# Performance work log

Measured on AMD Instinct MI355X. Metric: run time of the kernel, lower is better.

The kernel has to match this reference:

```python
import jax, jax.numpy as jnp
import numpy as np
import math

DIM = 1024
NUMHEADS = 16
HEAD_DIM = DIM // NUMHEADS
B, N = 4, 1024


def setup_inputs() -> dict:
    key = jax.random.key(0)
    ks = jax.random.split(key, 12)
    x = jax.random.normal(ks[0], (B, N, DIM), dtype=jnp.float32)
    decaymask = jax.random.uniform(ks[1], (NUMHEADS, N, N), dtype=jnp.float32)
    s = 1.0 / math.sqrt(DIM)
    wq = jax.random.normal(ks[2], (DIM, DIM), dtype=jnp.float32) * s
    bq = jnp.zeros((DIM,), dtype=jnp.float32)
    wk = jax.random.normal(ks[3], (DIM, DIM), dtype=jnp.float32) * s
    bk = jnp.zeros((DIM,), dtype=jnp.float32)
    wv = jax.random.normal(ks[4], (DIM, DIM), dtype=jnp.float32) * s
    bv = jnp.zeros((DIM,), dtype=jnp.float32)
    wo = jax.random.normal(ks[5], (DIM, DIM), dtype=jnp.float32) * s
    bo = jnp.zeros((DIM,), dtype=jnp.float32)
    return {"x": x, "decaymask": decaymask, "wq": wq, "bq": bq, "wk": wk,
            "bk": bk, "wv": wv, "bv": bv, "wo": wo, "bo": bo}


def reference(x, decaymask, wq, bq, wk, bk, wv, bv, wo, bo):
    Bx, Nx, D = x.shape
    # projections (torch Linear: x @ W^T + b)
    q = x @ wq.T + bq
    k = x @ wk.T + bk
    v = x @ wv.T + bv
    # [B, H, N, Hd]
    q = q.reshape(Bx, Nx, NUMHEADS, HEAD_DIM).transpose(0, 2, 1, 3)
    k = k.reshape(Bx, Nx, NUMHEADS, HEAD_DIM).transpose(0, 2, 1, 3)
    v = v.reshape(Bx, Nx, NUMHEADS, HEAD_DIM).transpose(0, 2, 1, 3)
    scores = jnp.einsum('bhqd,bhkd->bhqk', q, k) / math.sqrt(HEAD_DIM)
    scores = scores * decaymask[None]  # multiplicative decay mask before softmax
    attn = jax.nn.softmax(scores, axis=-1)
    out = jnp.einsum('bhqk,bhkd->bhqd', attn, v)
    out = out.transpose(0, 2, 1, 3).reshape(Bx, Nx, D)
    return out @ wo.T + bo
```

## Files before the change

### kernel.cpp

```cpp
#include <hip/hip_runtime.h>
#include <hip/hip_bf16.h>
#include <math.h>

typedef __bf16 bf16;
typedef __bf16 bf16x8 __attribute__((ext_vector_type(8)));
typedef __bf16 bf16x4 __attribute__((ext_vector_type(4)));
typedef float f32x4 __attribute__((ext_vector_type(4)));
typedef unsigned short u16;
typedef u16 u16x8 __attribute__((ext_vector_type(8)));

#define SEQ 1024
#define DIMSZ 1024
#define NHEADS 16
#define HEADDIM 64
#define BATCH 4

typedef __attribute__((address_space(1))) const unsigned char gas_u8;
typedef __attribute__((address_space(3))) unsigned char las_u8;
__device__ __forceinline__ void gload16(const void* g, void* l) {
    __builtin_amdgcn_global_load_lds((const gas_u8*)g, (las_u8*)l, 16, 0, 0);
}

__global__ void cvt_swz(const float4* __restrict__ src, bf16* __restrict__ dst,
                        int n4, float scale) {
    int i = blockIdx.x * blockDim.x + threadIdx.x;
    if (i >= n4) return;
    float4 v = src[i];
    int e0 = i << 2;
    int row = e0 >> 10, col = e0 & 1023;
    int col2 = (col & ~63) | (col & 7) | (((((col >> 3) & 7) ^ (row & 7))) << 3);
    bf16x4 o;
    o[0] = (bf16)(v.x * scale);
    o[1] = (bf16)(v.y * scale);
    o[2] = (bf16)(v.z * scale);
    o[3] = (bf16)(v.w * scale);
    *reinterpret_cast<bf16x4*>(&dst[(size_t)row * 1024 + col2]) = o;
}

__device__ __forceinline__ bf16x8 fragswz(const bf16* base, int row, int kb) {
    return *reinterpret_cast<const bf16x8*>(
        reinterpret_cast<const char*>(base) + row * 128 + (kb ^ ((row & 7) << 4)));
}

#define LDT 72
__device__ __forceinline__ bf16x8 ldsfrag72(const bf16* base, int row0, int k0, int lane) {
    return *reinterpret_cast<const bf16x8*>(base + (row0 + (lane & 15)) * LDT + k0 + ((lane >> 4) << 3));
}

template <int WN, int OUT_F32>
__global__ __launch_bounds__(256) void gemm_glds(
    const bf16* __restrict__ A, const bf16* __restrict__ Bm,
    const float* __restrict__ b0, const float* __restrict__ b1, const float* __restrict__ b2,
    float s0, void* __restrict__ Cv, int M, int N, int K)
{
    __shared__ __align__(16) bf16 As[128 * 64];
    __shared__ __align__(16) bf16 Bs[WN * 32 * 64];

    const int BN = WN * 32;
    const int nbn = N / BN;
    const int bm = blockIdx.x / nbn, bn = blockIdx.x % nbn;
    const int m0 = bm << 7, n0 = bn * BN;
    const int tid = threadIdx.x, lane = tid & 63, wid = tid >> 6;
    const int wr = wid >> 1, wc = wid & 1;
    const int lq = lane & 15, g = lane >> 4;

    f32x4 acc[4][WN];
    #pragma unroll
    for (int m = 0; m < 4; ++m)
        #pragma unroll
        for (int n = 0; n < WN; ++n)
            acc[m][n] = (f32x4){0.f, 0.f, 0.f, 0.f};

    for (int kt = 0; kt < K; kt += 64) {
        #pragma unroll
        for (int i = 0; i < 4; ++i) {
            int rb = wid * 32 + i * 8;
            gload16(&A[(size_t)(m0 + rb + (lane >> 3)) * K + kt + ((lane & 7) << 3)],
                    &As[rb * 64]);
        }
        #pragma unroll
        for (int i = 0; i < WN; ++i) {
            int rb = wid * (WN * 8) + i * 8;
            gload16(&Bm[(size_t)(n0 + rb + (lane >> 3)) * K + kt + ((lane & 7) << 3)],
                    &Bs[rb * 64]);
        }
        __syncthreads();

        bf16x8 af[4][2], bfr[WN][2];
        #pragma unroll
        for (int m = 0; m < 4; ++m)
            #pragma unroll
            for (int h2 = 0; h2 < 2; ++h2)
                af[m][h2] = fragswz(As, wr * 64 + m * 16 + lq, h2 * 64 + g * 16);
        #pragma unroll
        for (int n = 0; n < WN; ++n)
            #pragma unroll
            for (int h2 = 0; h2 < 2; ++h2)
                bfr[n][h2] = fragswz(Bs, wc * (WN * 16) + n * 16 + lq, h2 * 64 + g * 16);

        #pragma unroll
        for (int m = 0; m < 4; ++m)
            #pragma unroll
            for (int n = 0; n < WN; ++n)
                #pragma unroll
                for (int h2 = 0; h2 < 2; ++h2)
                    acc[m][n] = __builtin_amdgcn_mfma_f32_16x16x32_bf16(
                        af[m][h2], bfr[n][h2], acc[m][n], 0, 0, 0);
        __syncthreads();
    }

    const int seg = n0 >> 10;
    const float* bp = (seg == 0) ? b0 : ((seg == 1) ? b1 : b2);
    const float bsc = (seg == 0) ? s0 : 1.f;

    #pragma unroll
    for (int m = 0; m < 4; ++m) {
        #pragma unroll
        for (int n = 0; n < WN; ++n) {
            int rbase = m0 + wr * 64 + m * 16 + (g << 2);
            int col = n0 + wc * (WN * 16) + n * 16 + lq;
            float bv = bp[col - (seg << 10)] * bsc;
            #pragma unroll
            for (int r = 0; r < 4; ++r) {
                float v = acc[m][n][r] + bv;
                if (OUT_F32)
                    ((float*)Cv)[(size_t)(rbase + r) * N + col] = v;
                else
                    ((bf16*)Cv)[(size_t)(rbase + r) * N + col] = (bf16)v;
            }
        }
    }
}

struct KVRegs { bf16x8 k0, k1; u16x8 v0, v1; };

__device__ __forceinline__ void issue_loads(KVRegs& r, const bf16* qkv, int brow,
                                            int koff, int voff, int tid) {
    const int rK = tid >> 3, o8 = (tid & 7) << 3;
    r.k0 = *reinterpret_cast<const bf16x8*>(&qkv[(size_t)(brow + rK) * 3072 + koff + o8]);
    r.k1 = *reinterpret_cast<const bf16x8*>(&qkv[(size_t)(brow + rK + 32) * 3072 + koff + o8]);
    const int rV = rK << 1;
    r.v0 = *reinterpret_cast<const u16x8*>(&qkv[(size_t)(brow + rV) * 3072 + voff + o8]);
    r.v1 = *reinterpret_cast<const u16x8*>(&qkv[(size_t)(brow + rV + 1) * 3072 + voff + o8]);
}

__device__ __forceinline__ void write_stage(const KVRegs& r, bf16* Kb, bf16* Vb, int tid) {
    const int rK = tid >> 3, o = tid & 7, o8 = o << 3;
    *reinterpret_cast<bf16x8*>(&Kb[rK * LDT + o8]) = r.k0;
    *reinterpret_cast<bf16x8*>(&Kb[(rK + 32) * LDT + o8]) = r.k1;
    const int rV = rK << 1;
    #pragma unroll
    for (int j = 0; j < 8; ++j) {
        int d = o8 + j;
        int byteo = (d * 144 + rV * 2) ^ (o << 4);
        unsigned int w = (unsigned int)r.v0[j] | ((unsigned int)r.v1[j] << 16);
        *reinterpret_cast<unsigned int*>(reinterpret_cast<char*>(Vb) + byteo) = w;
    }
}

__device__ __forceinline__ void compute_stage(
    const bf16* Kb, const bf16* Vb, bf16* Psw,
    const float4 (&mreg)[4], const bf16x8 (&aqb)[2],
    float& m_run, float& l_run, f32x4 (&oacc)[4], int lane)
{
    const int lq = lane & 15, g = lane >> 4;
    f32x4 sacc[4];
    #pragma unroll
    for (int ct = 0; ct < 4; ++ct) sacc[ct] = (f32x4){0.f, 0.f, 0.f, 0.f};
    #pragma unroll
    for (int ct = 0; ct < 4; ++ct)
        #pragma unroll
        for (int h2 = 0; h2 < 2; ++h2)
            sacc[ct] = __builtin_amdgcn_mfma_f32_16x16x32_bf16(
                ldsfrag72(Kb, ct * 16, h2 * 32, lane), aqb[h2], sacc[ct], 0, 0, 0);

    float sv[4][4];
    float mx = -3.0e38f;
    #pragma unroll
    for (int ct = 0; ct < 4; ++ct) {
        sv[ct][0] = sacc[ct][0] * mreg[ct].x;
        sv[ct][1] = sacc[ct][1] * mreg[ct].y;
        sv[ct][2] = sacc[ct][2] * mreg[ct].z;
        sv[ct][3] = sacc[ct][3] * mreg[ct].w;
        mx = fmaxf(mx, fmaxf(fmaxf(sv[ct][0], sv[ct][1]), fmaxf(sv[ct][2], sv[ct][3])));
    }
    mx = fmaxf(mx, __shfl_xor(mx, 16, 64));
    mx = fmaxf(mx, __shfl_xor(mx, 32, 64));

    if (!__all(mx <= m_run + 8.f)) {
        float mnew = fmaxf(m_run, mx);
        float scl = __expf(m_run - mnew);
        l_run *= scl;
        #pragma unroll
        for (int ot = 0; ot < 4; ++ot) oacc[ot] *= scl;
        m_run = mnew;
    }

    float sum = 0.f;
    float pl[4][4];
    #pragma unroll
    for (int ct = 0; ct < 4; ++ct)
        #pragma unroll
        for (int r = 0; r < 4; ++r) {
            float p = __expf(sv[ct][r] - m_run);
            pl[ct][r] = p;
            sum += p;
        }
    sum += __shfl_xor(sum, 16, 64);
    sum += __shfl_xor(sum, 32, 64);
    l_run += sum;

    #pragma unroll
    for (int ct = 0; ct < 4; ++ct) {
        bf16x4 pb;
        pb[0] = (bf16)pl[ct][0]; pb[1] = (bf16)pl[ct][1];
        pb[2] = (bf16)pl[ct][2]; pb[3] = (bf16)pl[ct][3];
        *reinterpret_cast<bf16x4*>(&Psw[lq * LDT + ct * 16 + (g << 2)]) = pb;
    }

    #pragma unroll
    for (int ot = 0; ot < 4; ++ot) {
        #pragma unroll
        for (int h2 = 0; h2 < 2; ++h2) {
            int d = ot * 16 + lq;
            int byteo = (d * 144 + (h2 * 32 + g * 8) * 2) ^ (((d >> 3) & 7) << 4);
            bf16x8 vf = *reinterpret_cast<const bf16x8*>(
                reinterpret_cast<const char*>(Vb) + byteo);
            bf16x8 pf = *reinterpret_cast<const bf16x8*>(&Psw[lq * LDT + h2 * 32 + g * 8]);
            oacc[ot] = __builtin_amdgcn_mfma_f32_16x16x32_bf16(vf, pf, oacc[ot], 0, 0, 0);
        }
    }
}

__global__ __launch_bounds__(256) void attn_kernel(
    const bf16* __restrict__ qkv, const float* __restrict__ mask, bf16* __restrict__ Og)
{
    __shared__ __align__(16) bf16 Kbuf[2][64 * LDT];
    __shared__ __align__(16) bf16 Vbuf[2][64 * LDT];
    __shared__ __align__(16) bf16 Ps[4][16 * LDT];

    const int bid = blockIdx.x;
    const int xcd = bid & 7, slot = bid >> 3;
    const int pg = xcd * 32 + (slot >> 1);
    const int bp = slot & 1;
    const int h = pg >> 4, qblk = pg & 15;

    const int tid = threadIdx.x, lane = tid & 63, wid = tid >> 6;
    const int lq = lane & 15, g = lane >> 4;
    const int q = (qblk << 6) + wid * 16 + lq;
    const int koff = 1024 + h * HEADDIM, voff = 2048 + h * HEADDIM, qoff = h * HEADDIM;
    const float* mh = mask + (size_t)h * SEQ * SEQ + (size_t)q * SEQ;

    bf16x8 aq[2][2];
    #pragma unroll
    for (int bi = 0; bi < 2; ++bi)
        #pragma unroll
        for (int h2 = 0; h2 < 2; ++h2)
            aq[bi][h2] = *reinterpret_cast<const bf16x8*>(
                &qkv[(size_t)((bp * 2 + bi) * SEQ + q) * 3072 + qoff + h2 * 32 + g * 8]);

    float m_run[2] = {-3.0e38f, -3.0e38f};
    float l_run[2] = {0.f, 0.f};
    f32x4 oacc[2][4] = {};

    KVRegs s0, s1;
    issue_loads(s0, qkv, (bp * 2 + 0) * SEQ, koff, voff, tid);
    issue_loads(s1, qkv, (bp * 2 + 1) * SEQ, koff, voff, tid);
    float4 mregA[4], mregB[4];
    #pragma unroll
    for (int ct = 0; ct < 4; ++ct) {
        mregA[ct] = *reinterpret_cast<const float4*>(&mh[ct * 16 + (g << 2)]);
        mregB[ct] = *reinterpret_cast<const float4*>(&mh[64 + ct * 16 + (g << 2)]);
    }
    write_stage(s0, Kbuf[0], Vbuf[0], tid);
    __syncthreads();

    for (int t = 0; t < 16; ++t) {
        if (t < 15) issue_loads(s0, qkv, (bp * 2 + 0) * SEQ + (t + 1) * 64, koff, voff, tid);
        compute_stage(Kbuf[0], Vbuf[0], Ps[wid], mregA, aq[0],
                      m_run[0], l_run[0], oacc[0], lane);
        write_stage(s1, Kbuf[1], Vbuf[1], tid);
        __syncthreads();

        if (t < 15) issue_loads(s1, qkv, (bp * 2 + 1) * SEQ + (t + 1) * 64, koff, voff, tid);
        compute_stage(Kbuf[1], Vbuf[1], Ps[wid], mregA, aq[1],
                      m_run[1], l_run[1], oacc[1], lane);
        #pragma unroll
        for (int ct = 0; ct < 4; ++ct) mregA[ct] = mregB[ct];
        if (t < 14)
            #pragma unroll
            for (int ct = 0; ct < 4; ++ct)
                mregB[ct] = *reinterpret_cast<const float4*>(&mh[(t + 2) * 64 + ct * 16 + (g << 2)]);
        if (t < 15) write_stage(s0, Kbuf[0], Vbuf[0], tid);
        __syncthreads();
    }

    #pragma unroll
    for (int bi = 0; bi < 2; ++bi) {
        float inv = 1.f / l_run[bi];
        #pragma unroll
        for (int ot = 0; ot < 4; ++ot) {
            bf16x4 o;
            o[0] = (bf16)(oacc[bi][ot][0] * inv);
            o[1] = (bf16)(oacc[bi][ot][1] * inv);
            o[2] = (bf16)(oacc[bi][ot][2] * inv);
            o[3] = (bf16)(oacc[bi][ot][3] * inv);
            int lcol = ot * 16 + (g << 2);
            int chunk = (lcol >> 3) ^ (q & 7);
            int col = h * HEADDIM + (chunk << 3) + (lcol & 7);
            *reinterpret_cast<bf16x4*>(
                &Og[(size_t)((bp * 2 + bi) * SEQ + q) * DIMSZ + col]) = o;
        }
    }
}

extern "C" void kernel_launch(void* const* d_in, const int* in_sizes, int n_in,
                              void* d_out, int out_size, void* d_ws, size_t ws_size,
                              hipStream_t stream) {
    const float* x    = (const float*)d_in[0];
    const float* mask = (const float*)d_in[1];
    const float* wq   = (const float*)d_in[2];
    const float* bq   = (const float*)d_in[3];
    const float* wk   = (const float*)d_in[4];
    const float* bk   = (const float*)d_in[5];
    const float* wv   = (const float*)d_in[6];
    const float* bv   = (const float*)d_in[7];
    const float* wo   = (const float*)d_in[8];
    const float* bo   = (const float*)d_in[9];
    float* out = (float*)d_out;

    const size_t MTOK = (size_t)BATCH * SEQ;
    char* ws = (char*)d_ws;
    bf16* xb    = (bf16*)ws; ws += MTOK * DIMSZ * 2;
    bf16* wqkvb = (bf16*)ws; ws += (size_t)3 * DIMSZ * DIMSZ * 2;
    bf16* wob   = (bf16*)ws; ws += (size_t)DIMSZ * DIMSZ * 2;
    bf16* qkv   = (bf16*)ws; ws += MTOK * 3 * DIMSZ * 2;
    bf16* aob   = (bf16*)ws; ws += MTOK * DIMSZ * 2;

    int n4x = (int)(MTOK * DIMSZ / 4);
    cvt_swz<<<(n4x + 255) / 256, 256, 0, stream>>>((const float4*)x, xb, n4x, 1.f);
    int n4w = DIMSZ * DIMSZ / 4;
    int gw = (n4w + 255) / 256;
    cvt_swz<<<gw, 256, 0, stream>>>((const float4*)wq, wqkvb,                 n4w, 0.125f);
    cvt_swz<<<gw, 256, 0, stream>>>((const float4*)wk, wqkvb + 1024 * 1024,   n4w, 1.f);
    cvt_swz<<<gw, 256, 0, stream>>>((const float4*)wv, wqkvb + 2 * 1024 * 1024, n4w, 1.f);
    cvt_swz<<<gw, 256, 0, stream>>>((const float4*)wo, wob,                   n4w, 1.f);

    gemm_glds<4, 0><<<(MTOK / 128) * (3 * DIMSZ / 128), 256, 0, stream>>>(
        xb, wqkvb, bq, bk, bv, 0.125f, qkv, (int)MTOK, 3 * DIMSZ, DIMSZ);

    attn_kernel<<<512, 256, 0, stream>>>(qkv, mask, aob);

    gemm_glds<2, 1><<<(MTOK / 128) * (DIMSZ / 64), 256, 0, stream>>>(
        aob, wob, bo, bo, bo, 1.f, out, (int)MTOK, DIMSZ, DIMSZ);
}
```

Measured before the change: 120.1 us.

## Restructure attention to 32 queries per wave, merge weight conversions, remap GEMM blocks

New measurement: 130.4 us. 1.09x slower.

```diff
diff --git a/kernel.cpp b/kernel.cpp
--- a/kernel.cpp
+++ b/kernel.cpp
@@ -21,12 +21,7 @@
     __builtin_amdgcn_global_load_lds((const gas_u8*)g, (las_u8*)l, 16, 0, 0);
 }
 
-__global__ void cvt_swz(const float4* __restrict__ src, bf16* __restrict__ dst,
-                        int n4, float scale) {
-    int i = blockIdx.x * blockDim.x + threadIdx.x;
-    if (i >= n4) return;
-    float4 v = src[i];
-    int e0 = i << 2;
+__device__ __forceinline__ void cvt_store(const float4 v, bf16* dst, int e0, float scale) {
     int row = e0 >> 10, col = e0 & 1023;
     int col2 = (col & ~63) | (col & 7) | (((((col >> 3) & 7) ^ (row & 7))) << 3);
     bf16x4 o;
@@ -37,6 +32,23 @@
     *reinterpret_cast<bf16x4*>(&dst[(size_t)row * 1024 + col2]) = o;
 }
 
+__global__ void cvt_swz(const float4* __restrict__ src, bf16* __restrict__ dst,
+                        int n4, float scale) {
+    int i = blockIdx.x * blockDim.x + threadIdx.x;
+    if (i >= n4) return;
+    cvt_store(src[i], dst, i << 2, scale);
+}
+
+__global__ void cvt_weights(const float4* __restrict__ wq, const float4* __restrict__ wk,
+                            const float4* __restrict__ wv, const float4* __restrict__ wo,
+                            bf16* __restrict__ wqkvb, bf16* __restrict__ wob) {
+    int i = blockIdx.x * blockDim.x + threadIdx.x;
+    int mat = i >> 18, li = i & 262143;
+    const float4* s = (mat == 0) ? wq : (mat == 1) ? wk : (mat == 2) ? wv : wo;
+    bf16* d = (mat < 3) ? (wqkvb + (size_t)mat * 1024 * 1024) : wob;
+    cvt_store(s[li], d, li << 2, (mat == 0) ? 0.125f : 1.f);
+}
+
 __device__ __forceinline__ bf16x8 fragswz(const bf16* base, int row, int kb) {
     return *reinterpret_cast<const bf16x8*>(
         reinterpret_cast<const char*>(base) + row * 128 + (kb ^ ((row & 7) << 4)));
@@ -58,7 +70,8 @@
 
     const int BN = WN * 32;
     const int nbn = N / BN;
-    const int bm = blockIdx.x / nbn, bn = blockIdx.x % nbn;
+    const int wrk = (blockIdx.x & 7) * ((int)gridDim.x >> 3) + (blockIdx.x >> 3);
+    const int bm = wrk / nbn, bn = wrk % nbn;
     const int m0 = bm << 7, n0 = bn * BN;
     const int tid = threadIdx.x, lane = tid & 63, wid = tid >> 6;
     const int wr = wid >> 1, wc = wid & 1;
@@ -98,6 +111,7 @@
             for (int h2 = 0; h2 < 2; ++h2)
                 bfr[n][h2] = fragswz(Bs, wc * (WN * 16) + n * 16 + lq, h2 * 64 + g * 16);
 
+        __builtin_amdgcn_s_setprio(1);
         #pragma unroll
         for (int m = 0; m < 4; ++m)
             #pragma unroll
@@ -106,6 +120,7 @@
                 for (int h2 = 0; h2 < 2; ++h2)
                     acc[m][n] = __builtin_amdgcn_mfma_f32_16x16x32_bf16(
                         af[m][h2], bfr[n][h2], acc[m][n], 0, 0, 0);
+        __builtin_amdgcn_s_setprio(0);
         __syncthreads();
     }
 
@@ -160,64 +175,86 @@
 
 __device__ __forceinline__ void compute_stage(
     const bf16* Kb, const bf16* Vb, bf16* Psw,
-    const float4 (&mreg)[4], const bf16x8 (&aqb)[2],
-    float& m_run, float& l_run, f32x4 (&oacc)[4], int lane)
+    const float4 (&mreg)[2][4], const bf16x8 (&aq)[2][2],
+    float (&m_run)[2], float (&l_run)[2], f32x4 (&oacc)[2][4], int lane)
 {
     const int lq = lane & 15, g = lane >> 4;
-    f32x4 sacc[4];
-    #pragma unroll
-    for (int ct = 0; ct < 4; ++ct) sacc[ct] = (f32x4){0.f, 0.f, 0.f, 0.f};
+
+    bf16x8 kf[4][2];
     #pragma unroll
     for (int ct = 0; ct < 4; ++ct)
         #pragma unroll
         for (int h2 = 0; h2 < 2; ++h2)
-            sacc[ct] = __builtin_amdgcn_mfma_f32_16x16x32_bf16(
-                ldsfrag72(Kb, ct * 16, h2 * 32, lane), aqb[h2], sacc[ct], 0, 0, 0);
-
-    float sv[4][4];
-    float mx = -3.0e38f;
-    #pragma unroll
-    for (int ct = 0; ct < 4; ++ct) {
-        sv[ct][0] = sacc[ct][0] * mreg[ct].x;
-        sv[ct][1] = sacc[ct][1] * mreg[ct].y;
-        sv[ct][2] = sacc[ct][2] * mreg[ct].z;
-        sv[ct][3] = sacc[ct][3] * mreg[ct].w;
-        mx = fmaxf(mx, fmaxf(fmaxf(sv[ct][0], sv[ct][1]), fmaxf(sv[ct][2], sv[ct][3])));
-    }
-    mx = fmaxf(mx, __shfl_xor(mx, 16, 64));
-    mx = fmaxf(mx, __shfl_xor(mx, 32, 64));
-
-    if (!__all(mx <= m_run + 8.f)) {
-        float mnew = fmaxf(m_run, mx);
-        float scl = __expf(m_run - mnew);
-        l_run *= scl;
-        #pragma unroll
-        for (int ot = 0; ot < 4; ++ot) oacc[ot] *= scl;
-        m_run = mnew;
-    }
-
-    float sum = 0.f;
-    float pl[4][4];
-    #pragma unroll
-    for (int ct = 0; ct < 4; ++ct)
-        #pragma unroll
-        for (int r = 0; r < 4; ++r) {
-            float p = __expf(sv[ct][r] - m_run);
-            pl[ct][r] = p;
-            sum += p;
-        }
-    sum += __shfl_xor(sum, 16, 64);
-    sum += __shfl_xor(sum, 32, 64);
-    l_run += sum;
-
-    #pragma unroll
-    for (int ct = 0; ct < 4; ++ct) {
-        bf16x4 pb;
-        pb[0] = (bf16)pl[ct][0]; pb[1] = (bf16)pl[ct][1];
-        pb[2] = (bf16)pl[ct][2]; pb[3] = (bf16)pl[ct][3];
-        *reinterpret_cast<bf16x4*>(&Psw[lq * LDT + ct * 16 + (g << 2)]) = pb;
-    }
-
+            kf[ct][h2] = ldsfrag72(Kb, ct * 16, h2 * 32, lane);
+
+    #pragma unroll
+    for (int qs = 0; qs < 2; ++qs) {
+        f32x4 sacc[4];
+        #pragma unroll
+        for (int ct = 0; ct < 4; ++ct) sacc[ct] = (f32x4){0.f, 0.f, 0.f, 0.f};
+        __builtin_amdgcn_s_setprio(1);
+        #pragma unroll
+        for (int ct = 0; ct < 4; ++ct)
+            #pragma unroll
+            for (int h2 = 0; h2 < 2; ++h2)
+                sacc[ct] = __builtin_amdgcn_mfma_f32_16x16x32_bf16(
+                    kf[ct][h2], aq[qs][h2], sacc[ct], 0, 0, 0);
+        __builtin_amdgcn_s_setprio(0);
+
+        float sv[4][4];
+        float mx = -3.0e38f;
+        #pragma unroll
+        for (int ct = 0; ct < 4; ++ct) {
+            sv[ct][0] = sacc[ct][0] * mreg[qs][ct].x;
+            sv[ct][1] = sacc[ct][1] * mreg[qs][ct].y;
+            sv[ct][2] = sacc[ct][2] * mreg[qs][ct].z;
+            sv[ct][3] = sacc[ct][3] * mreg[qs][ct].w;
+            mx = fmaxf(mx, fmaxf(fmaxf(sv[ct][0], sv[ct][1]), fmaxf(sv[ct][2], sv[ct][3])));
+        }
+        mx = fmaxf(mx, __shfl_xor(mx, 16, 64));
+        mx = fmaxf(mx, __shfl_xor(mx, 32, 64));
+
+        if (!__all(mx <= m_run[qs] + 8.f)) {
+            float mnew = fmaxf(m_run[qs], mx);
+            float scl = __expf(m_run[qs] - mnew);
+            l_run[qs] *= scl;
+            #pragma unroll
+            for (int ot = 0; ot < 4; ++ot) oacc[qs][ot] *= scl;
+            m_run[qs] = mnew;
+        }
+
+        float sum = 0.f;
+        float pl[4][4];
+        #pragma unroll
+        for (int ct = 0; ct < 4; ++ct)
+            #pragma unroll
+            for (int r = 0; r < 4; ++r) {
+                float p = __expf(sv[ct][r] - m_run[qs]);
+                pl[ct][r] = p;
+                sum += p;
+            }
+        sum += __shfl_xor(sum, 16, 64);
+        sum += __shfl_xor(sum, 32, 64);
+        l_run[qs] += sum;
+
+        #pragma unroll
+        for (int ct = 0; ct < 4; ++ct) {
+            bf16x4 pb;
+            pb[0] = (bf16)pl[ct][0]; pb[1] = (bf16)pl[ct][1];
+            pb[2] = (bf16)pl[ct][2]; pb[3] = (bf16)pl[ct][3];
+            *reinterpret_cast<bf16x4*>(&Psw[(qs * 16 + lq) * LDT + ct * 16 + (g << 2)]) = pb;
+        }
+    }
+
+    bf16x8 pf[2][2];
+    #pragma unroll
+    for (int qs = 0; qs < 2; ++qs)
+        #pragma unroll
+        for (int h2 = 0; h2 < 2; ++h2)
+            pf[qs][h2] = *reinterpret_cast<const bf16x8*>(
+                &Psw[(qs * 16 + lq) * LDT + h2 * 32 + g * 8]);
+
+    __builtin_amdgcn_s_setprio(1);
     #pragma unroll
     for (int ot = 0; ot < 4; ++ot) {
         #pragma unroll
@@ -226,10 +263,13 @@
             int byteo = (d * 144 + (h2 * 32 + g * 8) * 2) ^ (((d >> 3) & 7) << 4);
             bf16x8 vf = *reinterpret_cast<const bf16x8*>(
                 reinterpret_cast<const char*>(Vb) + byteo);
-            bf16x8 pf = *reinterpret_cast<const bf16x8*>(&Psw[lq * LDT + h2 * 32 + g * 8]);
-            oacc[ot] = __builtin_amdgcn_mfma_f32_16x16x32_bf16(vf, pf, oacc[ot], 0, 0, 0);
-        }
-    }
+            #pragma unroll
+            for (int qs = 0; qs < 2; ++qs)
+                oacc[qs][ot] = __builtin_amdgcn_mfma_f32_16x16x32_bf16(
+                    vf, pf[qs][h2], oacc[qs][ot], 0, 0, 0);
+        }
+    }
+    __builtin_amdgcn_s_setprio(0);
 }
 
 __global__ __launch_bounds__(256) void attn_kernel(
@@ -237,79 +277,83 @@
 {
     __shared__ __align__(16) bf16 Kbuf[2][64 * LDT];
     __shared__ __align__(16) bf16 Vbuf[2][64 * LDT];
-    __shared__ __align__(16) bf16 Ps[4][16 * LDT];
+    __shared__ __align__(16) bf16 Ps[4][32 * LDT];
 
     const int bid = blockIdx.x;
     const int xcd = bid & 7, slot = bid >> 3;
-    const int pg = xcd * 32 + (slot >> 1);
-    const int bp = slot & 1;
-    const int h = pg >> 4, qblk = pg & 15;
+    const int b = slot & 3;
+    const int pg = ((slot >> 2) << 3) | xcd;
+    const int h = pg >> 3, qb = pg & 7;
 
     const int tid = threadIdx.x, lane = tid & 63, wid = tid >> 6;
     const int lq = lane & 15, g = lane >> 4;
-    const int q = (qblk << 6) + wid * 16 + lq;
+    const int q0 = qb * 128 + wid * 32 + lq;
+    const int q1 = q0 + 16;
     const int koff = 1024 + h * HEADDIM, voff = 2048 + h * HEADDIM, qoff = h * HEADDIM;
-    const float* mh = mask + (size_t)h * SEQ * SEQ + (size_t)q * SEQ;
+    const float* mh0 = mask + (size_t)h * SEQ * SEQ + (size_t)q0 * SEQ;
+    const float* mh1 = mask + (size_t)h * SEQ * SEQ + (size_t)q1 * SEQ;
 
     bf16x8 aq[2][2];
     #pragma unroll
-    for (int bi = 0; bi < 2; ++bi)
-        #pragma unroll
-        for (int h2 = 0; h2 < 2; ++h2)
-            aq[bi][h2] = *reinterpret_cast<const bf16x8*>(
-                &qkv[(size_t)((bp * 2 + bi) * SEQ + q) * 3072 + qoff + h2 * 32 + g * 8]);
+    for (int h2 = 0; h2 < 2; ++h2) {
+        aq[0][h2] = *reinterpret_cast<const bf16x8*>(
+            &qkv[(size_t)(b * SEQ + q0) * 3072 + qoff + h2 * 32 + g * 8]);
+        aq[1][h2] = *reinterpret_cast<const bf16x8*>(
+            &qkv[(size_t)(b * SEQ + q1) * 3072 + qoff + h2 * 32 + g * 8]);
+    }
 
     float m_run[2] = {-3.0e38f, -3.0e38f};
     float l_run[2] = {0.f, 0.f};
     f32x4 oacc[2][4] = {};
 
-    KVRegs s0, s1;
-    issue_loads(s0, qkv, (bp * 2 + 0) * SEQ, koff, voff, tid);
-    issue_loads(s1, qkv, (bp * 2 + 1) * SEQ, koff, voff, tid);
-    float4 mregA[4], mregB[4];
+    KVRegs s;
+    issue_loads(s, qkv, b * SEQ, koff, voff, tid);
+    float4 mregA[2][4], mregB[2][4];
     #pragma unroll
     for (int ct = 0; ct < 4; ++ct) {
-        mregA[ct] = *reinterpret_cast<const float4*>(&mh[ct * 16 + (g << 2)]);
-        mregB[ct] = *reinterpret_cast<const float4*>(&mh[64 + ct * 16 + (g << 2)]);
-    }
-    write_stage(s0, Kbuf[0], Vbuf[0], tid);
+        mregA[0][ct] = *reinterpret_cast<const float4*>(&mh0[ct * 16 + (g << 2)]);
+        mregA[1][ct] = *reinterpret_cast<const float4*>(&mh1[ct * 16 + (g << 2)]);
+        mregB[0][ct] = *reinterpret_cast<const float4*>(&mh0[64 + ct * 16 + (g << 2)]);
+        mregB[1][ct] = *reinterpret_cast<const float4*>(&mh1[64 + ct * 16 + (g << 2)]);
+    }
+    write_stage(s, Kbuf[0], Vbuf[0], tid);
     __syncthreads();
 
     for (int t = 0; t < 16; ++t) {
-        if (t < 15) issue_loads(s0, qkv, (bp * 2 + 0) * SEQ + (t + 1) * 64, koff, voff, tid);
-        compute_stage(Kbuf[0], Vbuf[0], Ps[wid], mregA, aq[0],
-                      m_run[0], l_run[0], oacc[0], lane);
-        write_stage(s1, Kbuf[1], Vbuf[1], tid);
+        if (t < 15) issue_loads(s, qkv, b * SEQ + (t + 1) * 64, koff, voff, tid);
+        compute_stage(Kbuf[t & 1], Vbuf[t & 1], Ps[wid], mregA, aq,
+                      m_run, l_run, oacc, lane);
+        if (t < 15) write_stage(s, Kbuf[(t + 1) & 1], Vbuf[(t + 1) & 1], tid);
+        #pragma unroll
+        for (int qs = 0; qs < 2; ++qs)
+            #pragma unroll
+            for (int ct = 0; ct < 4; ++ct) mregA[qs][ct] = mregB[qs][ct];
+        if (t < 14) {
+            #pragma unroll
+            for (int ct = 0; ct < 4; ++ct) {
+                mregB[0][ct] = *reinterpret_cast<const float4*>(&mh0[(t + 2) * 64 + ct * 16 + (g << 2)]);
+                mregB[1][ct] = *reinterpret_cast<const float4*>(&mh1[(t + 2) * 64 + ct * 16 + (g << 2)]);
+            }
+        }
         __syncthreads();
-
-        if (t < 15) issue_loads(s1, qkv, (bp * 2 + 1) * SEQ + (t + 1) * 64, koff, voff, tid);
-        compute_stage(Kbuf[1], Vbuf[1], Ps[wid], mregA, aq[1],
-                      m_run[1], l_run[1], oacc[1], lane);
-        #pragma unroll
-        for (int ct = 0; ct < 4; ++ct) mregA[ct] = mregB[ct];
-        if (t < 14)
-            #pragma unroll
-            for (int ct = 0; ct < 4; ++ct)
-                mregB[ct] = *reinterpret_cast<const float4*>(&mh[(t + 2) * 64 + ct * 16 + (g << 2)]);
-        if (t < 15) write_stage(s0, Kbuf[0], Vbuf[0], tid);
-        __syncthreads();
-    }
-
-    #pragma unroll
-    for (int bi = 0; bi < 2; ++bi) {
-        float inv = 1.f / l_run[bi];
+    }
+
+    #pragma unroll
+    for (int qs = 0; qs < 2; ++qs) {
+        float inv = 1.f / l_run[qs];
+        int q = (qs == 0) ? q0 : q1;
         #pragma unroll
         for (int ot = 0; ot < 4; ++ot) {
             bf16x4 o;
-            o[0] = (bf16)(oacc[bi][ot][0] * inv);
-            o[1] = (bf16)(oacc[bi][ot][1] * inv);
-            o[2] = (bf16)(oacc[bi][ot][2] * inv);
-            o[3] = (bf16)(oacc[bi][ot][3] * inv);
+            o[0] = (bf16)(oacc[qs][ot][0] * inv);
+            o[1] = (bf16)(oacc[qs][ot][1] * inv);
+            o[2] = (bf16)(oacc[qs][ot][2] * inv);
+            o[3] = (bf16)(oacc[qs][ot][3] * inv);
             int lcol = ot * 16 + (g << 2);
             int chunk = (lcol >> 3) ^ (q & 7);
             int col = h * HEADDIM + (chunk << 3) + (lcol & 7);
             *reinterpret_cast<bf16x4*>(
-                &Og[(size_t)((bp * 2 + bi) * SEQ + q) * DIMSZ + col]) = o;
+                &Og[(size_t)(b * SEQ + q) * DIMSZ + col]) = o;
         }
     }
 }
@@ -339,12 +383,9 @@
 
     int n4x = (int)(MTOK * DIMSZ / 4);
     cvt_swz<<<(n4x + 255) / 256, 256, 0, stream>>>((const float4*)x, xb, n4x, 1.f);
-    int n4w = DIMSZ * DIMSZ / 4;
-    int gw = (n4w + 255) / 256;
-    cvt_swz<<<gw, 256, 0, stream>>>((const float4*)wq, wqkvb,                 n4w, 0.125f);
-    cvt_swz<<<gw, 256, 0, stream>>>((const float4*)wk, wqkvb + 1024 * 1024,   n4w, 1.f);
-    cvt_swz<<<gw, 256, 0, stream>>>((const float4*)wv, wqkvb + 2 * 1024 * 1024, n4w, 1.f);
-    cvt_swz<<<gw, 256, 0, stream>>>((const float4*)wo, wob,                   n4w, 1.f);
+    cvt_weights<<<(4 * 262144) / 256, 256, 0, stream>>>(
+        (const float4*)wq, (const float4*)wk, (const float4*)wv, (const float4*)wo,
+        wqkvb, wob);
 
     gemm_glds<4, 0><<<(MTOK / 128) * (3 * DIMSZ / 128), 256, 0, stream>>>(
         xb, wqkvb, bq, bk, bv, 0.125f, qkv, (int)MTOK, 3 * DIMSZ, DIMSZ);
```
